# Performance work log

Measured on AMD Instinct MI355X. Metric: run time of the kernel, lower is better.

## Reference

```python
import jax, jax.numpy as jnp
import numpy as np

K = 4
TEMP = 0.5
PAD = 1

def setup_inputs() -> dict:
    key = jax.random.key(0)
    ks = jax.random.split(key, 5)
    B, C, H, W = 32, 256, 64, 64
    O, HID = 256, 65  # int(256*0.25)+1
    x = jax.random.normal(ks[0], (B, C, H, W), dtype=jnp.float32)
    w1 = jax.random.normal(ks[1], (HID, C), dtype=jnp.float32) * 0.05
    w2 = jax.random.normal(ks[2], (K * O, HID), dtype=jnp.float32) * 0.05
    b2 = jnp.zeros((K * O,), dtype=jnp.float32)
    weight = jax.random.normal(ks[3], (K, O, C, 3, 3), dtype=jnp.float32) * 0.05
    return {"x": x, "w1": w1, "w2": w2, "b2": b2, "weight": weight}

def _dyn_conv(x, w1, w2, b2, weight):
    B, C, H, W = x.shape
    Kk, O = weight.shape[0], weight.shape[1]
    # GPM2d attention: global avg pool -> 1x1 conv -> relu -> 1x1 conv -> softmax over K
    pooled = jnp.mean(x, axis=(2, 3))                     # [B, C]
    h = jax.nn.relu(pooled @ w1.T)                        # [B, HID]
    logits = (h @ w2.T + b2).reshape(B, Kk, O)            # [B, K, O]
    attn = jax.nn.softmax(logits / TEMP, axis=1)          # softmax over K experts
    # aggregate per-sample, per-out-channel weights: [B, O, C, k, k]
    agg_w = jnp.einsum('bko,kocij->bocij', attn, weight)
    # per-sample conv (equivalent to groups=batch trick in torch)
    def conv1(xi, wi):
        return jax.lax.conv_general_dilated(
            xi[None], wi, window_strides=(1, 1),
            padding=[(PAD, PAD), (PAD, PAD)],
            dimension_numbers=('NCHW', 'OIHW', 'NCHW'))[0]
    return jax.vmap(conv1)(x, agg_w)                      # [B, O, H, W]

def reference(x, w1, w2, b2, weight):
    return _dyn_conv(x, w1, w2, b2, weight)
```

## Files before the change

### kernel.cpp

```cpp
#include <hip/hip_runtime.h>
#include <stdint.h>

typedef unsigned short ushort_t;
typedef __attribute__((ext_vector_type(8))) short short8;
typedef __attribute__((ext_vector_type(4))) float floatx4;

#define B_    32
#define C_    256
#define O_    256
#define HID_  65
#define HW_   4096
#define KDIM  2304
#define XP_H  66
#define XPAD_ELEMS ((size_t)B_ * XP_H * XP_H * C_)
#define WAGG_ELEMS ((size_t)B_ * O_ * KDIM)

static __device__ __forceinline__ unsigned short f2bf(float f) {
  unsigned u = __float_as_uint(f);
  u += 0x7fffu + ((u >> 16) & 1u);
  return (unsigned short)(u >> 16);
}

static __device__ __forceinline__ void gld_lds16(const void* g, void* l) {
  __builtin_amdgcn_global_load_lds((__attribute__((address_space(1))) void*)(g),
                                   (__attribute__((address_space(3))) void*)(l),
                                   16, 0, 0);
}

__global__ void pool_kernel(const float* __restrict__ x, float* __restrict__ pooled) {
  const int lane = threadIdx.x & 63;
  const int wv   = threadIdx.x >> 6;
  const int bc   = blockIdx.x * 4 + wv;
  const float4* p = (const float4*)(x + (size_t)bc * HW_);
  float s = 0.f;
#pragma unroll
  for (int r = 0; r < 16; ++r) {
    float4 v = p[r * 64 + lane];
    s += v.x + v.y + v.z + v.w;
  }
#pragma unroll
  for (int off = 32; off; off >>= 1) s += __shfl_down(s, off, 64);
  if (lane == 0) pooled[bc] = s * (1.f / 4096.f);
}

__global__ void attn_kernel(const float* __restrict__ pooled,
                            const float* __restrict__ w1,
                            const float* __restrict__ w2,
                            const float* __restrict__ b2,
                            float* __restrict__ attn) {
  __shared__ float sp[C_];
  __shared__ float sh[HID_];
  const int b = blockIdx.x, t = threadIdx.x;
  sp[t] = pooled[b * C_ + t];
  __syncthreads();
  if (t < HID_) {
    float a = 0.f;
    for (int c = 0; c < C_; ++c) a += sp[c] * w1[t * C_ + c];
    sh[t] = fmaxf(a, 0.f);
  }
  __syncthreads();
  float lg[4];
#pragma unroll
  for (int k = 0; k < 4; ++k) {
    float a = b2[k * O_ + t];
    for (int j = 0; j < HID_; ++j) a += sh[j] * w2[(k * O_ + t) * HID_ + j];
    lg[k] = a * 2.0f;
  }
  float mx = fmaxf(fmaxf(lg[0], lg[1]), fmaxf(lg[2], lg[3]));
  float e0 = expf(lg[0] - mx), e1 = expf(lg[1] - mx);
  float e2 = expf(lg[2] - mx), e3 = expf(lg[3] - mx);
  float inv = 1.f / (e0 + e1 + e2 + e3);
  attn[(b * 4 + 0) * O_ + t] = e0 * inv;
  attn[(b * 4 + 1) * O_ + t] = e1 * inv;
  attn[(b * 4 + 2) * O_ + t] = e2 * inv;
  attn[(b * 4 + 3) * O_ + t] = e3 * inv;
}

__global__ void agg_kernel(const float* __restrict__ attn,
                           const float* __restrict__ wt,
                           ushort_t* __restrict__ wagg) {
  const int o = blockIdx.x;
  const int t = threadIdx.x;
  float wr[4][9];
#pragma unroll
  for (int k = 0; k < 4; ++k) {
    const float* src = wt + (size_t)(k * O_ + o) * KDIM + t * 9;
#pragma unroll
    for (int n = 0; n < 9; ++n) wr[k][n] = src[n];
  }
  for (int b = 0; b < B_; ++b) {
    const float a0 = attn[(b * 4 + 0) * O_ + o];
    const float a1 = attn[(b * 4 + 1) * O_ + o];
    const float a2 = attn[(b * 4 + 2) * O_ + o];
    const float a3 = attn[(b * 4 + 3) * O_ + o];
    ushort_t* dst = wagg + (size_t)(b * O_ + o) * KDIM;
#pragma unroll
    for (int n = 0; n < 9; ++n) {
      float v = a0 * wr[0][n] + a1 * wr[1][n] + a2 * wr[2][n] + a3 * wr[3][n];
      dst[n * C_ + t] = f2bf(v);
    }
  }
}

__global__ void pad_kernel(const float* __restrict__ x, ushort_t* __restrict__ xpad) {
  __shared__ float tile[64][65];
  const int hwT = blockIdx.x, cT = blockIdx.y, b = blockIdx.z;
  const int t = threadIdx.x;
  const int wl = t & 63, grp = t >> 6;
  const int hw0 = hwT * 64, c0 = cT * 64;
  const float* src = x + ((size_t)(b * C_ + c0)) * HW_ + hw0;
#pragma unroll
  for (int i = 0; i < 16; ++i) {
    const int ci = grp + i * 4;
    tile[ci][wl] = src[(size_t)ci * HW_ + wl];
  }
  __syncthreads();
  const int cp = (t & 31) * 2, g2 = t >> 5;
#pragma unroll
  for (int i = 0; i < 8; ++i) {
    const int hwi = g2 + i * 8;
    const int hw = hw0 + hwi;
    const int h = hw >> 6, w = hw & 63;
    ushort2 v;
    v.x = f2bf(tile[cp][hwi]);
    v.y = f2bf(tile[cp + 1][hwi]);
    *(ushort2*)(xpad + (((size_t)b * XP_H + (h + 1)) * XP_H + (w + 1)) * C_ + c0 + cp) = v;
  }
}

__global__ __launch_bounds__(256) void gemm_kernel(const ushort_t* __restrict__ xpad,
                                                   const ushort_t* __restrict__ wagg,
                                                   float* __restrict__ out) {
  __shared__ short lA[128 * 32];
  __shared__ short lB[128 * 32];

  const int hwT = blockIdx.x;
  const int oT  = blockIdx.y;
  const int b   = blockIdx.z;
  const int t    = threadIdx.x;
  const int lane = t & 63;
  const int wv   = t >> 6;

  const int hwBase = hwT << 7;
  const int h0     = hwT << 1;
  const int oBase  = oT << 7;

  const int rowIC = lane >> 2;
  const int slot  = lane & 3;
  const int cch   = slot ^ ((lane >> 3) & 3);

  size_t aG[2], bG[2];
  int ldsOff[2];
#pragma unroll
  for (int q = 0; q < 2; ++q) {
    const int chunk = wv * 2 + q;
    const int r = chunk * 16 + rowIC;
    aG[q] = (size_t)(b * O_ + oBase + r) * KDIM + cch * 8;
    const int hl = r >> 6, wl2 = r & 63;
    bG[q] = ((size_t)(b * XP_H + h0 + hl) * XP_H + wl2) * C_ + cch * 8;
    ldsOff[q] = chunk * 512;
  }

  const int lm   = lane & 15;
  const int quad = lane >> 4;
  const int mW = (wv & 1) << 6;
  const int nW = (wv >> 1) << 6;
  const int slotF = quad ^ ((lm >> 1) & 3);
  int aOff[4], bOff[4];
#pragma unroll
  for (int i = 0; i < 4; ++i) {
    aOff[i] = (mW + i * 16 + lm) * 32 + slotF * 8;
    bOff[i] = (nW + i * 16 + lm) * 32 + slotF * 8;
  }

  floatx4 acc[4][4] = {};

  for (int tap = 0; tap < 9; ++tap) {
    const int toff = (tap / 3) * XP_H + (tap % 3);
#pragma unroll 1
    for (int c0 = 0; c0 < C_; c0 += 32) {
      const int kk = tap * C_ + c0;
      __syncthreads();
#pragma unroll
      for (int q = 0; q < 2; ++q) {
        gld_lds16(wagg + aG[q] + kk, lA + ldsOff[q]);
        gld_lds16(xpad + bG[q] + (size_t)toff * C_ + c0, lB + ldsOff[q]);
      }
      __builtin_amdgcn_s_waitcnt(0x0f70);
      __syncthreads();

      short8 af[4], bf[4];
#pragma unroll
      for (int i = 0; i < 4; ++i) af[i] = *(const short8*)(lA + aOff[i]);
#pragma unroll
      for (int i = 0; i < 4; ++i) bf[i] = *(const short8*)(lB + bOff[i]);
#pragma unroll
      for (int mi = 0; mi < 4; ++mi)
#pragma unroll
        for (int ni = 0; ni < 4; ++ni)
          acc[mi][ni] = __builtin_amdgcn_mfma_f32_16x16x32_bf16(
              af[mi], bf[ni], acc[mi][ni], 0, 0, 0);
    }
  }

  const size_t outBase = (size_t)b * O_ * HW_;
#pragma unroll
  for (int mi = 0; mi < 4; ++mi) {
#pragma unroll
    for (int ni = 0; ni < 4; ++ni) {
      const int hw = hwBase + nW + ni * 16 + lm;
#pragma unroll
      for (int r = 0; r < 4; ++r) {
        const int o = oBase + mW + mi * 16 + quad * 4 + r;
        out[outBase + (size_t)o * HW_ + hw] = acc[mi][ni][r];
      }
    }
  }
}

extern "C" void kernel_launch(void* const* d_in, const int* in_sizes, int n_in,
                              void* d_out, int out_size, void* d_ws, size_t ws_size,
                              hipStream_t stream) {
  const float* x  = (const float*)d_in[0];
  const float* w1 = (const float*)d_in[1];
  const float* w2 = (const float*)d_in[2];
  const float* b2 = (const float*)d_in[3];
  const float* wt = (const float*)d_in[4];
  float* out = (float*)d_out;

  char* ws = (char*)d_ws;
  ushort_t* xpad = (ushort_t*)ws;
  ushort_t* wagg = (ushort_t*)(ws + XPAD_ELEMS * 2);
  float* pooled  = (float*)(ws + XPAD_ELEMS * 2 + WAGG_ELEMS * 2);
  float* attn    = pooled + B_ * C_;

  hipMemsetAsync(xpad, 0, XPAD_ELEMS * 2, stream);
  pool_kernel<<<2048, 256, 0, stream>>>(x, pooled);
  attn_kernel<<<B_, 256, 0, stream>>>(pooled, w1, w2, b2, attn);
  agg_kernel<<<O_, 256, 0, stream>>>(attn, wt, wagg);
  pad_kernel<<<dim3(64, 4, B_), 256, 0, stream>>>(x, xpad);
  gemm_kernel<<<dim3(32, 2, B_), 256, 0, stream>>>(xpad, wagg, out);
}
```

Baseline: 499.1 us.

## Fuse pooling into pad kernel, zero only borders, double GEMM K-step

The separate pooling pass over x is removed. The transpose/pad kernel now writes per-tile channel partial sums, and the attention kernel reduces those partials. The full memset of the padded buffer is replaced by a small kernel that zeroes only the border rows and columns. The GEMM loads 64 channels per LDS stage instead of 32, with a new XOR swizzle, which halves the number of barrier/load rounds at the cost of more shared memory per block.

```diff
diff --git a/kernel.cpp b/kernel.cpp
--- a/kernel.cpp
+++ b/kernel.cpp
@@ -27,23 +27,55 @@
                                    16, 0, 0);
 }
 
-__global__ void pool_kernel(const float* __restrict__ x, float* __restrict__ pooled) {
-  const int lane = threadIdx.x & 63;
-  const int wv   = threadIdx.x >> 6;
-  const int bc   = blockIdx.x * 4 + wv;
-  const float4* p = (const float4*)(x + (size_t)bc * HW_);
-  float s = 0.f;
-#pragma unroll
-  for (int r = 0; r < 16; ++r) {
-    float4 v = p[r * 64 + lane];
-    s += v.x + v.y + v.z + v.w;
-  }
-#pragma unroll
-  for (int off = 32; off; off >>= 1) s += __shfl_down(s, off, 64);
-  if (lane == 0) pooled[bc] = s * (1.f / 4096.f);
-}
-
-__global__ void attn_kernel(const float* __restrict__ pooled,
+__global__ void border_kernel(ushort_t* __restrict__ xpad) {
+  const int b = blockIdx.x, t = threadIdx.x;
+  uint4 z = {0u, 0u, 0u, 0u};
+  uint4* base = (uint4*)(xpad + (size_t)b * XP_H * XP_H * C_);
+  for (int i = t; i < 2112; i += 256) {
+    base[i] = z;
+    base[(size_t)65 * 2112 + i] = z;
+  }
+  for (int i = t; i < 64 * 32; i += 256) {
+    const int h = 1 + (i >> 5), s = i & 31;
+    base[(size_t)h * 2112 + s] = z;
+    base[(size_t)h * 2112 + 65 * 32 + s] = z;
+  }
+}
+
+__global__ void pad_kernel(const float* __restrict__ x, ushort_t* __restrict__ xpad,
+                           float* __restrict__ partial) {
+  __shared__ float tile[64][65];
+  const int hwT = blockIdx.x, cT = blockIdx.y, b = blockIdx.z;
+  const int t = threadIdx.x;
+  const int wl = t & 63, grp = t >> 6;
+  const int hw0 = hwT * 64, c0 = cT * 64;
+  const float* src = x + ((size_t)(b * C_ + c0)) * HW_ + hw0;
+#pragma unroll
+  for (int i = 0; i < 16; ++i) {
+    const int ci = grp + i * 4;
+    tile[ci][wl] = src[(size_t)ci * HW_ + wl];
+  }
+  __syncthreads();
+  if (t < 64) {
+    float s = 0.f;
+#pragma unroll
+    for (int i = 0; i < 64; ++i) s += tile[t][i];
+    partial[(size_t)hwT * (B_ * C_) + b * C_ + c0 + t] = s;
+  }
+  const int cp = (t & 31) * 2, g2 = t >> 5;
+#pragma unroll
+  for (int i = 0; i < 8; ++i) {
+    const int hwi = g2 + i * 8;
+    const int hw = hw0 + hwi;
+    const int h = hw >> 6, w = hw & 63;
+    ushort2 v;
+    v.x = f2bf(tile[cp][hwi]);
+    v.y = f2bf(tile[cp + 1][hwi]);
+    *(ushort2*)(xpad + (((size_t)b * XP_H + (h + 1)) * XP_H + (w + 1)) * C_ + c0 + cp) = v;
+  }
+}
+
+__global__ void attn_kernel(const float* __restrict__ partial,
                             const float* __restrict__ w1,
                             const float* __restrict__ w2,
                             const float* __restrict__ b2,
@@ -51,7 +83,12 @@
   __shared__ float sp[C_];
   __shared__ float sh[HID_];
   const int b = blockIdx.x, t = threadIdx.x;
-  sp[t] = pooled[b * C_ + t];
+  {
+    float s = 0.f;
+#pragma unroll
+    for (int i = 0; i < 64; ++i) s += partial[(size_t)i * (B_ * C_) + b * C_ + t];
+    sp[t] = s * (1.f / 4096.f);
+  }
   __syncthreads();
   if (t < HID_) {
     float a = 0.f;
@@ -102,37 +139,11 @@
   }
 }
 
-__global__ void pad_kernel(const float* __restrict__ x, ushort_t* __restrict__ xpad) {
-  __shared__ float tile[64][65];
-  const int hwT = blockIdx.x, cT = blockIdx.y, b = blockIdx.z;
-  const int t = threadIdx.x;
-  const int wl = t & 63, grp = t >> 6;
-  const int hw0 = hwT * 64, c0 = cT * 64;
-  const float* src = x + ((size_t)(b * C_ + c0)) * HW_ + hw0;
-#pragma unroll
-  for (int i = 0; i < 16; ++i) {
-    const int ci = grp + i * 4;
-    tile[ci][wl] = src[(size_t)ci * HW_ + wl];
-  }
-  __syncthreads();
-  const int cp = (t & 31) * 2, g2 = t >> 5;
-#pragma unroll
-  for (int i = 0; i < 8; ++i) {
-    const int hwi = g2 + i * 8;
-    const int hw = hw0 + hwi;
-    const int h = hw >> 6, w = hw & 63;
-    ushort2 v;
-    v.x = f2bf(tile[cp][hwi]);
-    v.y = f2bf(tile[cp + 1][hwi]);
-    *(ushort2*)(xpad + (((size_t)b * XP_H + (h + 1)) * XP_H + (w + 1)) * C_ + c0 + cp) = v;
-  }
-}
-
 __global__ __launch_bounds__(256) void gemm_kernel(const ushort_t* __restrict__ xpad,
                                                    const ushort_t* __restrict__ wagg,
                                                    float* __restrict__ out) {
-  __shared__ short lA[128 * 32];
-  __shared__ short lB[128 * 32];
+  __shared__ short lA[128 * 64];
+  __shared__ short lB[128 * 64];
 
   const int hwT = blockIdx.x;
   const int oT  = blockIdx.y;
@@ -145,61 +156,64 @@
   const int h0     = hwT << 1;
   const int oBase  = oT << 7;
 
-  const int rowIC = lane >> 2;
-  const int slot  = lane & 3;
-  const int cch   = slot ^ ((lane >> 3) & 3);
-
-  size_t aG[2], bG[2];
-  int ldsOff[2];
-#pragma unroll
-  for (int q = 0; q < 2; ++q) {
-    const int chunk = wv * 2 + q;
-    const int r = chunk * 16 + rowIC;
-    aG[q] = (size_t)(b * O_ + oBase + r) * KDIM + cch * 8;
-    const int hl = r >> 6, wl2 = r & 63;
-    bG[q] = ((size_t)(b * XP_H + h0 + hl) * XP_H + wl2) * C_ + cch * 8;
-    ldsOff[q] = chunk * 512;
+  const int rS = lane >> 3;
+  const int pS = lane & 7;
+  size_t aG[4], bG[4];
+  int ldsOff[4];
+#pragma unroll
+  for (int q = 0; q < 4; ++q) {
+    const int row = wv * 32 + q * 8 + rS;
+    const int lch = pS ^ (row & 7);
+    aG[q] = (size_t)(b * O_ + oBase + row) * KDIM + lch * 8;
+    const int hl = row >> 6, wl2 = row & 63;
+    bG[q] = ((size_t)(b * XP_H + h0 + hl) * XP_H + wl2) * C_ + lch * 8;
+    ldsOff[q] = (wv * 32 + q * 8) * 64;
   }
 
   const int lm   = lane & 15;
   const int quad = lane >> 4;
   const int mW = (wv & 1) << 6;
   const int nW = (wv >> 1) << 6;
-  const int slotF = quad ^ ((lm >> 1) & 3);
-  int aOff[4], bOff[4];
-#pragma unroll
-  for (int i = 0; i < 4; ++i) {
-    aOff[i] = (mW + i * 16 + lm) * 32 + slotF * 8;
-    bOff[i] = (nW + i * 16 + lm) * 32 + slotF * 8;
-  }
+  int aOff[2][4], bOff[2][4];
+#pragma unroll
+  for (int h = 0; h < 2; ++h)
+#pragma unroll
+    for (int i = 0; i < 4; ++i) {
+      const int ps = ((h * 4 + quad) ^ (lm & 7)) * 8;
+      aOff[h][i] = (mW + i * 16 + lm) * 64 + ps;
+      bOff[h][i] = (nW + i * 16 + lm) * 64 + ps;
+    }
 
   floatx4 acc[4][4] = {};
 
   for (int tap = 0; tap < 9; ++tap) {
     const int toff = (tap / 3) * XP_H + (tap % 3);
 #pragma unroll 1
-    for (int c0 = 0; c0 < C_; c0 += 32) {
+    for (int c0 = 0; c0 < C_; c0 += 64) {
       const int kk = tap * C_ + c0;
       __syncthreads();
 #pragma unroll
-      for (int q = 0; q < 2; ++q) {
+      for (int q = 0; q < 4; ++q) {
         gld_lds16(wagg + aG[q] + kk, lA + ldsOff[q]);
         gld_lds16(xpad + bG[q] + (size_t)toff * C_ + c0, lB + ldsOff[q]);
       }
       __builtin_amdgcn_s_waitcnt(0x0f70);
       __syncthreads();
 
-      short8 af[4], bf[4];
-#pragma unroll
-      for (int i = 0; i < 4; ++i) af[i] = *(const short8*)(lA + aOff[i]);
-#pragma unroll
-      for (int i = 0; i < 4; ++i) bf[i] = *(const short8*)(lB + bOff[i]);
-#pragma unroll
-      for (int mi = 0; mi < 4; ++mi)
-#pragma unroll
-        for (int ni = 0; ni < 4; ++ni)
-          acc[mi][ni] = __builtin_amdgcn_mfma_f32_16x16x32_bf16(
-              af[mi], bf[ni], acc[mi][ni], 0, 0, 0);
+#pragma unroll
+      for (int h = 0; h < 2; ++h) {
+        short8 af[4], bf[4];
+#pragma unroll
+        for (int i = 0; i < 4; ++i) af[i] = *(const short8*)(lA + aOff[h][i]);
+#pragma unroll
+        for (int i = 0; i < 4; ++i) bf[i] = *(const short8*)(lB + bOff[h][i]);
+#pragma unroll
+        for (int mi = 0; mi < 4; ++mi)
+#pragma unroll
+          for (int ni = 0; ni < 4; ++ni)
+            acc[mi][ni] = __builtin_amdgcn_mfma_f32_16x16x32_bf16(
+                af[mi], bf[ni], acc[mi][ni], 0, 0, 0);
+      }
     }
   }
 
@@ -231,13 +245,12 @@
   char* ws = (char*)d_ws;
   ushort_t* xpad = (ushort_t*)ws;
   ushort_t* wagg = (ushort_t*)(ws + XPAD_ELEMS * 2);
-  float* pooled  = (float*)(ws + XPAD_ELEMS * 2 + WAGG_ELEMS * 2);
-  float* attn    = pooled + B_ * C_;
-
-  hipMemsetAsync(xpad, 0, XPAD_ELEMS * 2, stream);
-  pool_kernel<<<2048, 256, 0, stream>>>(x, pooled);
-  attn_kernel<<<B_, 256, 0, stream>>>(pooled, w1, w2, b2, attn);
+  float* partial = (float*)(ws + XPAD_ELEMS * 2 + WAGG_ELEMS * 2);
+  float* attn    = partial + 64 * B_ * C_;
+
+  border_kernel<<<B_, 256, 0, stream>>>(xpad);
+  pad_kernel<<<dim3(64, 4, B_), 256, 0, stream>>>(x, xpad, partial);
+  attn_kernel<<<B_, 256, 0, stream>>>(partial, w1, w2, b2, attn);
   agg_kernel<<<O_, 256, 0, stream>>>(attn, wt, wagg);
-  pad_kernel<<<dim3(64, 4, B_), 256, 0, stream>>>(x, xpad);
   gemm_kernel<<<dim3(32, 2, B_), 256, 0, stream>>>(xpad, wagg, out);
 }
```

New measurement: 446.8 us. -10.5%, faster.
